# Optimization experiments

Measured on AMD Instinct MI355X. Metric: run time of the kernel, lower is better.

Reference implementation:

```python
import jax, jax.numpy as jnp
import numpy as np

FEATURE_DIM = 128

def setup_inputs() -> dict:
    key0 = jax.random.key(0)
    k1, k2, k3 = jax.random.split(key0, 3)
    B, NQ, NK, D = 4, 4096, 4096, FEATURE_DIM
    return {
        "target": jax.random.normal(k1, (B, NQ, D), dtype=jnp.float32),
        "key": jax.random.normal(k2, (B, NK, D), dtype=jnp.float32),
        "value": jax.random.normal(k3, (B, NK, D), dtype=jnp.float32),
    }

def reference(target, key, value):
    # Lan_K F: scores = target @ key^T / sqrt(d); weights = softmax(scores); out = weights @ value
    scale = 1.0 / np.sqrt(FEATURE_DIM).astype(np.float32)
    scores = jnp.einsum('bqd,bkd->bqk', target, key) * scale  # [B, NQ, NK]
    weights = jax.nn.softmax(scores, axis=-1)
    return jnp.einsum('bqk,bkd->bqd', weights, value)  # [B, NQ, D]
```

## Files before the change

### kernel.cpp

```cpp
#include <hip/hip_runtime.h>
#include <stdint.h>

#define B_ 4
#define NQ_ 4096
#define NK_ 4096
#define D_ 128
#define BM_ 64
#define BN_ 128
#define NITER_ (NK_/BN_)
#define PS_ 136
#define OS_ 66

typedef __attribute__((ext_vector_type(8))) short short8;
typedef __attribute__((ext_vector_type(4))) float floatx4;
typedef unsigned int u32;

union frag_u { u32 u[4]; short8 s; };
union pair_u { u32 u[2]; uint2 v; };

__device__ __forceinline__ unsigned short f2bf_rne(float x){
  union { float f; u32 u; } c; c.f = x;
  u32 u = c.u;
  return (unsigned short)((u + 0x7fffu + ((u >> 16) & 1u)) >> 16);
}
__device__ __forceinline__ u32 pk2bf(float a, float b){
  union { float f; u32 u; } x, y; x.f = a; y.f = b;
  return ((x.u + 0x8000u) >> 16) | ((y.u + 0x8000u) & 0xffff0000u);
}

#define TS_ 136
__global__ void prep_kernel(const float* __restrict__ k, const float* __restrict__ v,
                            unsigned short* __restrict__ kb, unsigned short* __restrict__ vt){
  if (blockIdx.x >= 256){
    int base = (blockIdx.x - 256) * 2048 + threadIdx.x;
    #pragma unroll
    for (int i = 0; i < 8; i++){
      int j = base + i*256;
      float4 val = ((const float4*)k)[j];
      ushort4 s;
      s.x = f2bf_rne(val.x); s.y = f2bf_rne(val.y);
      s.z = f2bf_rne(val.z); s.w = f2bf_rne(val.w);
      ((ushort4*)kb)[j] = s;
    }
    return;
  }
  __shared__ __align__(16) float tile[64*TS_];
  int blk = blockIdx.x; int b = blk >> 6; int kt = blk & 63; int k0 = kt*64;
  int t = threadIdx.x;
  const float* vb = v + ((size_t)b*NK_ + k0)*D_;
  #pragma unroll
  for (int i=0;i<8;i++){
    int f = t + i*256;
    int row = f >> 5, c4 = f & 31;
    *(float4*)(tile + row*TS_ + c4*4) = *(const float4*)(vb + row*D_ + c4*4);
  }
  __syncthreads();
  unsigned short* vtb = vt + (size_t)b*D_*NK_ + k0;
  #pragma unroll
  for (int i=0;i<16;i++){
    int u2 = t + i*256;
    int d = u2 >> 5, kp = u2 & 31;
    ushort2 s2;
    s2.x = f2bf_rne(tile[(2*kp)*TS_ + d]);
    s2.y = f2bf_rne(tile[(2*kp+1)*TS_ + d]);
    *(ushort2*)(vtb + (size_t)d*NK_ + 2*kp) = s2;
  }
}

__global__ __launch_bounds__(512, 2) void attn_kernel(
    const float* __restrict__ Qf, const unsigned short* __restrict__ Kb,
    const unsigned short* __restrict__ Vt, float* __restrict__ Out){
  __shared__ __align__(16) char sm[69632];
  unsigned short* smP = (unsigned short*)sm;
  float* smO = (float*)sm;
  float* smL = (float*)(sm + 67584);

  const int bi = blockIdx.x;
  const int b  = (bi >> 1) & 3;
  const int qt = ((bi >> 3) << 1) | (bi & 1);
  const int q0 = qt * BM_;
  const int tid = threadIdx.x;
  const int w = tid >> 6, lane = tid & 63;
  const int kg = w >> 1, dh = w & 1;
  const int l15 = lane & 15, l4 = lane >> 4;

  const unsigned short* kgb = Kb + (size_t)b * NK_ * D_;
  const unsigned short* vgb = Vt + (size_t)b * D_ * NK_;

  const unsigned short* kRow =
      kgb + (size_t)(kg*32 + (l15>>2)*8 + dh*4 + (l15&3)) * D_ + l4*8;
  const unsigned short* vBase = vgb + kg*32 + l4*8;

  short8 kf[4], knf[4];
  #pragma unroll
  for (int j = 0; j < 4; j++) kf[j] = *(const short8*)(kRow + j*32);

  short8 qf[4][4];
  {
    const float* qp = Qf + ((size_t)b*NQ_ + q0)*D_;
    #pragma unroll
    for (int nb = 0; nb < 4; nb++)
      #pragma unroll
      for (int kb = 0; kb < 4; kb++){
        const float* p = qp + (size_t)(nb*16 + l15)*D_ + kb*32 + l4*8;
        float4 a = *(const float4*)p;
        float4 c4 = *(const float4*)(p + 4);
        frag_u f;
        f.u[0] = pk2bf(a.x, a.y);  f.u[1] = pk2bf(a.z, a.w);
        f.u[2] = pk2bf(c4.x, c4.y); f.u[3] = pk2bf(c4.z, c4.w);
        qf[nb][kb] = f.s;
      }
  }

  floatx4 o[4][4];
  #pragma unroll
  for (int nb = 0; nb < 4; nb++)
    #pragma unroll
    for (int dt = 0; dt < 4; dt++) o[nb][dt] = (floatx4)0.0f;
  float lsum[4] = {0.f, 0.f, 0.f, 0.f};

  const float SL = 0.08838834764831845f * 1.4426950408889634f;

  for (int it = 0; it < NITER_; ++it){
    short8 vf[4];
    const unsigned short* vit = vBase + (size_t)it * BN_;
    #pragma unroll
    for (int dt = 0; dt < 4; dt++){
      int d = dh*64 + dt*16 + l15;
      vf[dt] = *(const short8*)(vit + (size_t)d * NK_);
    }
    if (it + 1 < NITER_){
      const unsigned short* kp = kRow + (size_t)(it+1) * (BN_ * D_);
      #pragma unroll
      for (int j = 0; j < 4; j++) knf[j] = *(const short8*)(kp + j*32);
    }

    floatx4 s[4];
    #pragma unroll
    for (int nb = 0; nb < 4; nb++){
      s[nb] = (floatx4)0.0f;
      s[nb] = __builtin_amdgcn_mfma_f32_16x16x32_bf16(kf[0], qf[nb][0], s[nb], 0,0,0);
      s[nb] = __builtin_amdgcn_mfma_f32_16x16x32_bf16(kf[1], qf[nb][1], s[nb], 0,0,0);
      s[nb] = __builtin_amdgcn_mfma_f32_16x16x32_bf16(kf[2], qf[nb][2], s[nb], 0,0,0);
      s[nb] = __builtin_amdgcn_mfma_f32_16x16x32_bf16(kf[3], qf[nb][3], s[nb], 0,0,0);
    }

    unsigned short* smPb = smP + (it & 1) * (64 * PS_);
    #pragma unroll
    for (int nb = 0; nb < 4; nb++){
      float p0 = __builtin_amdgcn_exp2f(s[nb][0] * SL);
      float p1 = __builtin_amdgcn_exp2f(s[nb][1] * SL);
      float p2 = __builtin_amdgcn_exp2f(s[nb][2] * SL);
      float p3 = __builtin_amdgcn_exp2f(s[nb][3] * SL);
      lsum[nb] += (p0 + p1) + (p2 + p3);
      pair_u pp; pp.u[0] = pk2bf(p0, p1); pp.u[1] = pk2bf(p2, p3);
      *(uint2*)(smPb + (size_t)(nb*16 + l15)*PS_ + kg*32 + l4*8 + dh*4) = pp.v;
    }

    __syncthreads();

    short8 pf[4];
    #pragma unroll
    for (int nb = 0; nb < 4; nb++)
      pf[nb] = *(const short8*)(smPb + (size_t)(nb*16 + l15)*PS_ + kg*32 + l4*8);
    #pragma unroll
    for (int nb = 0; nb < 4; nb++)
      #pragma unroll
      for (int dt = 0; dt < 4; dt++)
        o[nb][dt] = __builtin_amdgcn_mfma_f32_16x16x32_bf16(pf[nb], vf[dt], o[nb][dt], 0,0,0);

    #pragma unroll
    for (int j = 0; j < 4; j++) kf[j] = knf[j];
  }

  #pragma unroll
  for (int nb = 0; nb < 4; nb++){
    float v = lsum[nb];
    v += __shfl_xor(v, 16);
    v += __shfl_xor(v, 32);
    lsum[nb] = v;
  }
  if (l4 == 0)
    #pragma unroll
    for (int nb = 0; nb < 4; nb++)
      smL[w*64 + nb*16 + l15] = lsum[nb];

  __syncthreads();

  if (w >= 4){
    float* r = smO + (size_t)(w - 4) * 4224;
    #pragma unroll
    for (int nb = 0; nb < 4; nb++)
      #pragma unroll
      for (int dt = 0; dt < 4; dt++)
        #pragma unroll
        for (int q = 0; q < 4; q++)
          r[(size_t)(nb*16 + l4*4 + q)*OS_ + dt*16 + l15] = o[nb][dt][q];
  }
  __syncthreads();
  if (w < 4){
    float* r = smO + (size_t)w * 4224;
    #pragma unroll
    for (int nb = 0; nb < 4; nb++)
      #pragma unroll
      for (int dt = 0; dt < 4; dt++)
        #pragma unroll
        for (int q = 0; q < 4; q++)
          o[nb][dt][q] += r[(size_t)(nb*16 + l4*4 + q)*OS_ + dt*16 + l15];
  }
  __syncthreads();
  if (w == 2 || w == 3){
    float* r = smO + (size_t)(w - 2) * 4224;
    #pragma unroll
    for (int nb = 0; nb < 4; nb++)
      #pragma unroll
      for (int dt = 0; dt < 4; dt++)
        #pragma unroll
        for (int q = 0; q < 4; q++)
          r[(size_t)(nb*16 + l4*4 + q)*OS_ + dt*16 + l15] = o[nb][dt][q];
  }
  __syncthreads();
  if (w < 2){
    float* r = smO + (size_t)w * 4224;
    float* og = Out + ((size_t)b*NQ_ + q0)*D_ + dh*64;
    #pragma unroll
    for (int nb = 0; nb < 4; nb++)
      #pragma unroll
      for (int q = 0; q < 4; q++){
        int row = nb*16 + l4*4 + q;
        float lt = 0.f;
        #pragma unroll
        for (int w2 = 0; w2 < 8; w2++) lt += smL[w2*64 + row];
        float inv = 1.0f / lt;
        #pragma unroll
        for (int dt = 0; dt < 4; dt++){
          float val = o[nb][dt][q] + r[(size_t)row*OS_ + dt*16 + l15];
          og[(size_t)row*D_ + dt*16 + l15] = val * inv;
        }
      }
  }
}

extern "C" void kernel_launch(void* const* d_in, const int* in_sizes, int n_in,
                              void* d_out, int out_size, void* d_ws, size_t ws_size,
                              hipStream_t stream){
  const float* q = (const float*)d_in[0];
  const float* k = (const float*)d_in[1];
  const float* v = (const float*)d_in[2];
  float* out = (float*)d_out;
  unsigned short* kb = (unsigned short*)d_ws;
  unsigned short* vt = kb + (size_t)B_*NK_*D_;
  prep_kernel<<<512, 256, 0, stream>>>(k, v, kb, vt);
  attn_kernel<<<256, 512, 0, stream>>>(q, kb, vt, out);
}
```

Measured before the change: 141.5 us.

## Pre-swizzle K and V into per-lane MFMA fragment order for coalesced loads

Measured after the change: 120.5 us. 1.17x faster.

```diff
diff --git a/kernel.cpp b/kernel.cpp
--- a/kernel.cpp
+++ b/kernel.cpp
@@ -30,22 +30,33 @@
 
 #define TS_ 136
 __global__ void prep_kernel(const float* __restrict__ k, const float* __restrict__ v,
-                            unsigned short* __restrict__ kb, unsigned short* __restrict__ vt){
+                            unsigned short* __restrict__ kf, unsigned short* __restrict__ vf){
   if (blockIdx.x >= 256){
-    int base = (blockIdx.x - 256) * 2048 + threadIdx.x;
-    #pragma unroll
-    for (int i = 0; i < 8; i++){
-      int j = base + i*256;
-      float4 val = ((const float4*)k)[j];
-      ushort4 s;
-      s.x = f2bf_rne(val.x); s.y = f2bf_rne(val.y);
-      s.z = f2bf_rne(val.z); s.w = f2bf_rne(val.w);
-      ((ushort4*)kb)[j] = s;
+    int base = (blockIdx.x - 256) * 1024 + threadIdx.x;
+    #pragma unroll
+    for (int i = 0; i < 4; i++){
+      int flat = base + i*256;
+      int lane = flat & 63, j = (flat>>6)&3, w = (flat>>8)&7;
+      int it = (flat>>11)&31, b = flat>>16;
+      int kg = w>>1, dh = w&1, l15 = lane&15, l4 = lane>>4;
+      int key = it*128 + kg*32 + ((l15>>2)<<3) + dh*4 + (l15&3);
+      int d0 = j*32 + l4*8;
+      const float* p = k + ((size_t)b*NK_ + key)*D_ + d0;
+      float4 a = *(const float4*)p;
+      float4 c = *(const float4*)(p + 4);
+      ushort4 s0, s1;
+      s0.x = f2bf_rne(a.x); s0.y = f2bf_rne(a.y);
+      s0.z = f2bf_rne(a.z); s0.w = f2bf_rne(a.w);
+      s1.x = f2bf_rne(c.x); s1.y = f2bf_rne(c.y);
+      s1.z = f2bf_rne(c.z); s1.w = f2bf_rne(c.w);
+      ushort4* dst = (ushort4*)(kf + (size_t)flat*8);
+      dst[0] = s0; dst[1] = s1;
     }
     return;
   }
   __shared__ __align__(16) float tile[64*TS_];
   int blk = blockIdx.x; int b = blk >> 6; int kt = blk & 63; int k0 = kt*64;
+  int it = kt >> 1; int khalf = (kt & 1) * 64;
   int t = threadIdx.x;
   const float* vb = v + ((size_t)b*NK_ + k0)*D_;
   #pragma unroll
@@ -55,15 +66,19 @@
     *(float4*)(tile + row*TS_ + c4*4) = *(const float4*)(vb + row*D_ + c4*4);
   }
   __syncthreads();
-  unsigned short* vtb = vt + (size_t)b*D_*NK_ + k0;
   #pragma unroll
   for (int i=0;i<16;i++){
     int u2 = t + i*256;
     int d = u2 >> 5, kp = u2 & 31;
+    int klocal = khalf + 2*kp;
+    int kg = klocal >> 5, l4 = (klocal >> 3) & 3, ko7 = klocal & 7;
+    int dh = d >> 6, dt = (d >> 4) & 3, l15 = d & 15;
+    int w = kg*2 + dh, lane = l4*16 + l15;
+    size_t flat = ((((size_t)b*32 + it)*8 + w)*4 + dt)*64 + lane;
     ushort2 s2;
     s2.x = f2bf_rne(tile[(2*kp)*TS_ + d]);
     s2.y = f2bf_rne(tile[(2*kp+1)*TS_ + d]);
-    *(ushort2*)(vtb + (size_t)d*NK_ + 2*kp) = s2;
+    *(ushort2*)(vf + flat*8 + ko7) = s2;
   }
 }
 
@@ -84,16 +99,14 @@
   const int kg = w >> 1, dh = w & 1;
   const int l15 = lane & 15, l4 = lane >> 4;
 
-  const unsigned short* kgb = Kb + (size_t)b * NK_ * D_;
-  const unsigned short* vgb = Vt + (size_t)b * D_ * NK_;
-
-  const unsigned short* kRow =
-      kgb + (size_t)(kg*32 + (l15>>2)*8 + dh*4 + (l15&3)) * D_ + l4*8;
-  const unsigned short* vBase = vgb + kg*32 + l4*8;
+  const short8* Kfrag = (const short8*)Kb;
+  const short8* Vfrag = (const short8*)Vt;
+  const size_t FSTRIDE = 8*4*64;
+  const size_t fbase = (((size_t)b*32)*8 + w)*4*64 + lane;
 
   short8 kf[4], knf[4];
   #pragma unroll
-  for (int j = 0; j < 4; j++) kf[j] = *(const short8*)(kRow + j*32);
+  for (int j = 0; j < 4; j++) kf[j] = Kfrag[fbase + j*64];
 
   short8 qf[4][4];
   {
@@ -123,16 +136,13 @@
 
   for (int it = 0; it < NITER_; ++it){
     short8 vf[4];
-    const unsigned short* vit = vBase + (size_t)it * BN_;
-    #pragma unroll
-    for (int dt = 0; dt < 4; dt++){
-      int d = dh*64 + dt*16 + l15;
-      vf[dt] = *(const short8*)(vit + (size_t)d * NK_);
-    }
+    #pragma unroll
+    for (int dt = 0; dt < 4; dt++)
+      vf[dt] = Vfrag[fbase + (size_t)it*FSTRIDE + dt*64];
     if (it + 1 < NITER_){
-      const unsigned short* kp = kRow + (size_t)(it+1) * (BN_ * D_);
-      #pragma unroll
-      for (int j = 0; j < 4; j++) knf[j] = *(const short8*)(kp + j*32);
+      #pragma unroll
+      for (int j = 0; j < 4; j++)
+        knf[j] = Kfrag[fbase + (size_t)(it+1)*FSTRIDE + j*64];
     }
 
     floatx4 s[4];
```
